# Performance work log

Hardware: AMD Instinct MI355X
Metric: run time of the kernel (lower is better)

The kernel has to match this reference:

```python
import jax, jax.numpy as jnp
import numpy as np

N = 50000
E0 = 800000
IN_CH = 128
HID = 64
OUT_CH = 64
HEADS = 2
NEG_SLOPE = 0.2


def _xavier(key, shape):
    fan_in, fan_out = shape[-2], shape[-1]
    limit = (6.0 / (fan_in + fan_out)) ** 0.5
    return jax.random.uniform(key, shape, jnp.float32, -limit, limit)


def setup_inputs() -> dict:
    key = jax.random.key(0)
    ks = jax.random.split(key, 10)
    x = jax.random.normal(ks[0], (N, IN_CH), jnp.float32)
    src = jax.random.randint(ks[1], (E0,), 0, N)
    dst = jax.random.randint(ks[2], (E0,), 0, N)
    dst = jnp.where(src == dst, (dst + 1) % N, dst)  # no self loops in input
    edge_index = jnp.stack([src, dst]).astype(jnp.int64)
    emb_w = _xavier(ks[3], (HID, IN_CH))
    emb_b = jnp.zeros((HID,), jnp.float32)
    # layer 0: in=HID, out=HID, heads=HEADS
    w0 = _xavier(ks[4], (HEADS, HID, HID))
    a0 = _xavier(ks[5], (1, HEADS, 2 * HID))
    # layer 1: in=HEADS*HID, out=HID, heads=HEADS
    w1 = _xavier(ks[6], (HEADS, HEADS * HID, HID))
    a1 = _xavier(ks[7], (1, HEADS, 2 * HID))
    # layer 2: in=HEADS*HID, out=OUT_CH, heads=1, concat=False
    w2 = _xavier(ks[8], (1, HEADS * HID, OUT_CH))
    a2 = _xavier(ks[9], (1, 1, 2 * OUT_CH))
    return {"x": x, "edge_index": edge_index, "emb_w": emb_w, "emb_b": emb_b,
            "w0": w0, "a0": a0, "w1": w1, "a1": a1, "w2": w2, "a2": a2}


def gat_layer(x, w, a, src, dst, concat):
    # x: [N, F_in]; w: [H, F_in, C]; a: [1, H, 2C]; src/dst: [E]
    C = w.shape[-1]
    xh = jnp.einsum('nf,hfc->nhc', x, w)               # [N, H, C]
    a_i, a_j = a[0, :, :C], a[0, :, C:]                # each [H, C]
    # (cat(x_i, x_j) * a).sum(-1) == <x_i, a_i> + <x_j, a_j>; compute per node then gather
    s_i = jnp.einsum('nhc,hc->nh', xh, a_i)            # [N, H]
    s_j = jnp.einsum('nhc,hc->nh', xh, a_j)            # [N, H]
    alpha = jax.nn.leaky_relu(s_i[dst] + s_j[src], NEG_SLOPE)  # [E, H]
    # segment softmax over destination nodes
    m = jax.ops.segment_max(alpha, dst, num_segments=N)
    alpha = jnp.exp(alpha - m[dst])
    denom = jax.ops.segment_sum(alpha, dst, num_segments=N)
    alpha = alpha / (denom[dst] + 1e-16)
    out = jax.ops.segment_sum(xh[src] * alpha[:, :, None], dst, num_segments=N)  # [N, H, C]
    if concat:
        return out.reshape(N, -1)
    return out.mean(axis=1)


def _forward(x, edge_index, emb_w, emb_b, w0, a0, w1, a1, w2, a2):
    # add self loops (inputs contain none, matching remove+add in the source)
    loop = jnp.arange(N, dtype=edge_index.dtype)
    src = jnp.concatenate([edge_index[0], loop])
    dst = jnp.concatenate([edge_index[1], loop])
    h = x @ emb_w.T + emb_b                            # nn.Linear embedding
    h = jax.nn.elu(gat_layer(h, w0, a0, src, dst, True))
    h = jax.nn.elu(gat_layer(h, w1, a1, src, dst, True))
    h = jax.nn.elu(gat_layer(h, w2, a2, src, dst, False))
    return h


def reference(x, edge_index, emb_w, emb_b, w0, a0, w1, a1, w2, a2):
    return _forward(x, edge_index, emb_w, emb_b, w0, a0, w1, a1, w2, a2)
```

## Files before the change

### kernel.cpp

```cpp
#include <hip/hip_runtime.h>
#include <math.h>

typedef __attribute__((ext_vector_type(8))) short short8v;
typedef __attribute__((ext_vector_type(4))) float float4v;

union uf32 { unsigned int u; float f; };

__device__ __forceinline__ unsigned short f2b(float f) {
  uf32 v; v.f = f;
  unsigned int u = v.u;
  return (unsigned short)((u + 0x7fffu + ((u >> 16) & 1u)) >> 16);
}

__global__ void zero8(int* __restrict__ p, int n) {
  int i = blockIdx.x * 256 + threadIdx.x;
  if (i < n) p[i] = 0;
}

__global__ void hist8(const int* __restrict__ ei, int* __restrict__ cnt8,
                      unsigned short* __restrict__ lpos, int E0, int N) {
  int e = blockIdx.x * 256 + threadIdx.x;
  if (e >= E0 + N) return;
  int vx = blockIdx.x & 7;
  int d = (e < E0) ? ei[E0 + e] : (e - E0);
  lpos[e] = (unsigned short)atomicAdd(&cnt8[vx * N + d], 1);
}

__global__ void fold8(const int* __restrict__ cnt8, int* __restrict__ base8,
                      int* __restrict__ cnt, int* __restrict__ part, int N) {
  __shared__ int lds[256];
  int d = blockIdx.x * 256 + threadIdx.x;
  int run = 0;
  if (d < N) {
#pragma unroll
    for (int x = 0; x < 8; ++x) {
      int t = cnt8[x * N + d];
      base8[x * N + d] = run;
      run += t;
    }
    cnt[d] = run;
  }
  lds[threadIdx.x] = (d < N) ? run : 0;
  __syncthreads();
  for (int o = 128; o; o >>= 1) {
    if (threadIdx.x < o) lds[threadIdx.x] += lds[threadIdx.x + o];
    __syncthreads();
  }
  if (threadIdx.x == 0) part[blockIdx.x] = lds[0];
}

__global__ void scan_carry(int* __restrict__ part, int nb) {
  __shared__ int lds[256];
  __shared__ int carry;
  if (threadIdx.x == 0) carry = 0;
  __syncthreads();
  for (int t0 = 0; t0 < nb; t0 += 256) {
    int t = t0 + threadIdx.x;
    int v = (t < nb) ? part[t] : 0;
    lds[threadIdx.x] = v;
    __syncthreads();
    for (int o = 1; o < 256; o <<= 1) {
      int x = (threadIdx.x >= o) ? lds[threadIdx.x - o] : 0;
      __syncthreads();
      lds[threadIdx.x] += x;
      __syncthreads();
    }
    if (t < nb) part[t] = carry + lds[threadIdx.x] - v;
    __syncthreads();
    if (threadIdx.x == 255) carry += lds[255];
    __syncthreads();
  }
}

__global__ void scan3(const int* __restrict__ cnt, const int* __restrict__ part,
                      const int* __restrict__ base8, int* __restrict__ rp,
                      int* __restrict__ rb8, int N, int E) {
  __shared__ int lds[256];
  int t = threadIdx.x;
  int idx = blockIdx.x * 256 + t;
  int v = (idx < N) ? cnt[idx] : 0;
  lds[t] = v;
  __syncthreads();
  for (int o = 1; o < 256; o <<= 1) {
    int x = (t >= o) ? lds[t - o] : 0;
    __syncthreads();
    lds[t] += x;
    __syncthreads();
  }
  if (idx < N) {
    const int rpv = part[blockIdx.x] + lds[t] - v;
    rp[idx] = rpv;
#pragma unroll
    for (int x = 0; x < 8; ++x) rb8[x * N + idx] = rpv + base8[x * N + idx];
  }
  if (blockIdx.x == 0 && t == 0) rp[N] = E;
}

__global__ void fillx(const int* __restrict__ ei, const int* __restrict__ rb8,
                      const unsigned short* __restrict__ lpos,
                      int* __restrict__ col, int E0, int N) {
  int e = blockIdx.x * 256 + threadIdx.x;
  if (e >= E0 + N) return;
  int vx = blockIdx.x & 7;
  int s, d;
  if (e < E0) { s = ei[e]; d = ei[E0 + e]; }
  else        { s = e - E0; d = s; }
  col[rb8[vx * N + d] + lpos[e]] = s;
}

__global__ void pack_all(const float* __restrict__ emb_w, const float* __restrict__ w0,
                         const float* __restrict__ w1, const float* __restrict__ w2,
                         unsigned short* __restrict__ pE, unsigned short* __restrict__ p0,
                         unsigned short* __restrict__ p1, unsigned short* __restrict__ p2) {
  int b = blockIdx.x;
  const float* w; unsigned short* bp;
  int F, sf, sc, h;
  if (b < 32)       { w = emb_w; bp = pE; F = 128; sf = 1;  sc = 128; h = 0; }
  else if (b < 64)  { b -= 32;  w = w0; bp = p0; F = 64;  sf = 64; sc = 1; h = b / 16; b %= 16; }
  else if (b < 128) { b -= 64;  w = w1; bp = p1; F = 128; sf = 64; sc = 1; h = b / 32; b %= 32; }
  else              { b -= 128; w = w2; bp = p2; F = 128; sf = 64; sc = 1; h = 0; }
  int i = b * 256 + threadIdx.x;
  if (i >= F * 64) return;
  int j = i & 7, colc = (i >> 3) & 15, g = (i >> 7) & 3, ct = (i >> 9) & 3, kk = i >> 11;
  int f = kk * 32 + g * 8 + j;
  int c = ct * 16 + colc;
  float v = w[(size_t)h * F * 64 + (size_t)f * sf + (size_t)c * sc];
  bp[(size_t)h * F * 64 + i] = f2b(v);
}

template <int F, int H, bool SCORES, bool BIAS, bool IBF, bool OBF>
__global__ __launch_bounds__(256) void gemm_mfma(
    const void* __restrict__ in, const unsigned short* __restrict__ bp,
    const float* __restrict__ bias, const float* __restrict__ a,
    void* __restrict__ xh_out, float* __restrict__ si, float* __restrict__ sj,
    int nrows) {
  constexpr int SA = F + 8;
  constexpr int NK = F / 32;
  constexpr int HC = H * 64;
  __shared__ __align__(16) unsigned short A_lds[64 * SA];

  const int tid = threadIdx.x;
  const int lane = tid & 63;
  const int wv = tid >> 6;
  const int n0 = blockIdx.x * 64;

  if (IBF) {
    const unsigned short* inb = (const unsigned short*)in;
    constexpr int NCH = 64 * F / 8;
#pragma unroll
    for (int i0 = 0; i0 < NCH; i0 += 256) {
      const int i = i0 + tid;
      const int row = i / (F / 8);
      const int c8 = i % (F / 8);
      int rg = n0 + row;
      if (rg >= nrows) rg = nrows - 1;
      const short8v v = *reinterpret_cast<const short8v*>(inb + (size_t)rg * F + c8 * 8);
      *reinterpret_cast<short8v*>(A_lds + row * SA + c8 * 8) = v;
    }
  } else {
    const float* inf = (const float*)in;
    constexpr int NCH = 64 * F / 4;
#pragma unroll
    for (int i0 = 0; i0 < NCH; i0 += 256) {
      const int i = i0 + tid;
      const int row = i / (F / 4);
      const int c4 = i % (F / 4);
      int rg = n0 + row;
      if (rg >= nrows) rg = nrows - 1;
      const float4 v = *reinterpret_cast<const float4*>(inf + (size_t)rg * F + c4 * 4);
      unsigned short* d = A_lds + row * SA + c4 * 4;
      d[0] = f2b(v.x); d[1] = f2b(v.y); d[2] = f2b(v.z); d[3] = f2b(v.w);
    }
  }
  __syncthreads();

  const int g = lane >> 4;
  const int cl = lane & 15;

  short8v af[NK];
  const unsigned short* ar = A_lds + (wv * 16 + cl) * SA + g * 8;
#pragma unroll
  for (int kk = 0; kk < NK; ++kk) af[kk] = *reinterpret_cast<const short8v*>(ar + kk * 32);

#pragma unroll
  for (int h = 0; h < H; ++h) {
    const unsigned short* __restrict__ bph = bp + (size_t)h * (F * 64);

    float4v acc[4];
#pragma unroll
    for (int ct = 0; ct < 4; ++ct) acc[ct] = (float4v){0.f, 0.f, 0.f, 0.f};

#pragma unroll
    for (int kk = 0; kk < NK; ++kk) {
#pragma unroll
      for (int ct = 0; ct < 4; ++ct) {
        const short8v bf = *reinterpret_cast<const short8v*>(
            bph + ((size_t)((kk * 4 + ct) * 4 + g)) * 128 + cl * 8);
        acc[ct] = __builtin_amdgcn_mfma_f32_16x16x32_bf16(af[kk], bf, acc[ct], 0, 0, 0);
      }
    }

    if (BIAS) {
#pragma unroll
      for (int ct = 0; ct < 4; ++ct) {
        const float b = bias[ct * 16 + cl];
#pragma unroll
        for (int reg = 0; reg < 4; ++reg) acc[ct][reg] += b;
      }
    }

#pragma unroll
    for (int ct = 0; ct < 4; ++ct) {
      const int c = ct * 16 + cl;
#pragma unroll
      for (int reg = 0; reg < 4; ++reg) {
        const int n = n0 + wv * 16 + g * 4 + reg;
        if (n < nrows) {
          const size_t idx = (size_t)n * HC + h * 64 + c;
          if (OBF) ((unsigned short*)xh_out)[idx] = f2b(acc[ct][reg]);
          else     ((float*)xh_out)[idx] = acc[ct][reg];
        }
      }
    }

    if (SCORES) {
      float pi[4] = {0.f, 0.f, 0.f, 0.f}, pj[4] = {0.f, 0.f, 0.f, 0.f};
#pragma unroll
      for (int ct = 0; ct < 4; ++ct) {
        const float av = a[h * 128 + ct * 16 + cl];
        const float bv = a[h * 128 + 64 + ct * 16 + cl];
#pragma unroll
        for (int reg = 0; reg < 4; ++reg) {
          pi[reg] = fmaf(acc[ct][reg], av, pi[reg]);
          pj[reg] = fmaf(acc[ct][reg], bv, pj[reg]);
        }
      }
#pragma unroll
      for (int reg = 0; reg < 4; ++reg) {
#pragma unroll
        for (int o = 8; o; o >>= 1) {
          pi[reg] += __shfl_xor(pi[reg], o, 64);
          pj[reg] += __shfl_xor(pj[reg], o, 64);
        }
      }
      if (cl == 0) {
#pragma unroll
        for (int reg = 0; reg < 4; ++reg) {
          const int n = n0 + wv * 16 + g * 4 + reg;
          if (n < nrows) {
            si[(size_t)n * H + h] = pi[reg];
            sj[(size_t)n * H + h] = pj[reg];
          }
        }
      }
    }
  }
}

template <int H, bool OBF>
__global__ __launch_bounds__(256) void agg_kernel(
    const unsigned short* __restrict__ xh, const float* __restrict__ si_g,
    const float* __restrict__ sj_g, const int* __restrict__ rp,
    const int* __restrict__ col, void* __restrict__ out, int N) {
  constexpr int HC = H * 64;
  const int lane = threadIdx.x & 63;
  const int n = blockIdx.x * 4 + (threadIdx.x >> 6);
  if (n >= N) return;
  const int el = lane & 31;
  const int hl = (H == 2) ? (lane >> 5) : 0;

  const int base = rp[n];
  const int deg = rp[n + 1] - base;
  const float siv = si_g[(size_t)n * H + hl];

  const int soff = (H == 1) ? (lane >> 5) : 0;
  const int qoff = (H == 1) ? (lane >> 5) : (lane & 32);
  constexpr int STEP = (H == 2) ? 1 : 2;
  const unsigned int loff = (H == 2) ? (unsigned)lane * 2 : (unsigned)el * 2;

  float m = 0.f, den = 0.f, acc0 = 0.f, acc1 = 0.f;

  for (int start = 0; start < deg; start += 32) {
    const int k = start + el;
    const bool vld = k < deg;
    const int s = vld ? col[base + k] : 0;
    float al = -INFINITY;
    if (vld) {
      const float t = siv + sj_g[(size_t)s * H + hl];
      al = (t > 0.f) ? t : 0.2f * t;
    }
    float cm = al;
#pragma unroll
    for (int o = 16; o; o >>= 1) cm = fmaxf(cm, __shfl_xor(cm, o, 64));
    if (start == 0) {
      m = cm;
    } else {
      const float nm = fmaxf(m, cm);
      const float r = __expf(m - nm);
      den *= r; acc0 *= r; acc1 *= r; m = nm;
    }
    const float p = vld ? __expf(al - m) : 0.f;
    float ps = p;
#pragma unroll
    for (int o = 16; o; o >>= 1) ps += __shfl_xor(ps, o, 64);
    den += ps;

    const int cc = min(32, deg - start);
    int kk = 0;
    for (; kk + 8 * STEP <= cc; kk += 8 * STEP) {
      int sb[8]; float qb[8]; unsigned int uv[8];
#pragma unroll
      for (int u = 0; u < 8; ++u) {
        const int e = kk + u * STEP;
        sb[u] = __shfl(s, e + soff, 64);
        qb[u] = __shfl(p, e + qoff, 64);
      }
#pragma unroll
      for (int u = 0; u < 8; ++u)
        uv[u] = *reinterpret_cast<const unsigned int*>(xh + (size_t)sb[u] * HC + loff);
#pragma unroll
      for (int u = 0; u < 8; ++u) {
        uf32 lo, hi;
        lo.u = uv[u] << 16;
        hi.u = uv[u] & 0xffff0000u;
        acc0 = fmaf(qb[u], lo.f, acc0);
        acc1 = fmaf(qb[u], hi.f, acc1);
      }
    }
    for (; kk + 4 * STEP <= cc; kk += 4 * STEP) {
      int sb[4]; float qb[4]; unsigned int uv[4];
#pragma unroll
      for (int u = 0; u < 4; ++u) {
        const int e = kk + u * STEP;
        sb[u] = __shfl(s, e + soff, 64);
        qb[u] = __shfl(p, e + qoff, 64);
      }
#pragma unroll
      for (int u = 0; u < 4; ++u)
        uv[u] = *reinterpret_cast<const unsigned int*>(xh + (size_t)sb[u] * HC + loff);
#pragma unroll
      for (int u = 0; u < 4; ++u) {
        uf32 lo, hi;
        lo.u = uv[u] << 16;
        hi.u = uv[u] & 0xffff0000u;
        acc0 = fmaf(qb[u], lo.f, acc0);
        acc1 = fmaf(qb[u], hi.f, acc1);
      }
    }
    for (; kk < cc; kk += STEP) {
      const int sb = __shfl(s, kk + soff, 64);
      const float qb = __shfl(p, kk + qoff, 64);
      const unsigned int uv = *reinterpret_cast<const unsigned int*>(xh + (size_t)sb * HC + loff);
      uf32 lo, hi;
      lo.u = uv << 16;
      hi.u = uv & 0xffff0000u;
      acc0 = fmaf(qb, lo.f, acc0);
      acc1 = fmaf(qb, hi.f, acc1);
    }
  }

  if (H == 2) {
    const float invd = 1.f / (den + 1e-16f);
    float v0 = acc0 * invd, v1 = acc1 * invd;
    v0 = (v0 > 0.f) ? v0 : expm1f(v0);
    v1 = (v1 > 0.f) ? v1 : expm1f(v1);
    if (OBF) {
      unsigned int pk = ((unsigned int)f2b(v1) << 16) | (unsigned int)f2b(v0);
      *reinterpret_cast<unsigned int*>((unsigned short*)out + (size_t)n * 128 + lane * 2) = pk;
    } else {
      float2 o; o.x = v0; o.y = v1;
      *reinterpret_cast<float2*>((float*)out + (size_t)n * 128 + lane * 2) = o;
    }
  } else {
    acc0 += __shfl_xor(acc0, 32, 64);
    acc1 += __shfl_xor(acc1, 32, 64);
    if (lane < 32) {
      const float invd = 1.f / (den + 1e-16f);
      float v0 = acc0 * invd, v1 = acc1 * invd;
      v0 = (v0 > 0.f) ? v0 : expm1f(v0);
      v1 = (v1 > 0.f) ? v1 : expm1f(v1);
      if (OBF) {
        unsigned int pk = ((unsigned int)f2b(v1) << 16) | (unsigned int)f2b(v0);
        *reinterpret_cast<unsigned int*>((unsigned short*)out + (size_t)n * 64 + el * 2) = pk;
      } else {
        float2 o; o.x = v0; o.y = v1;
        *reinterpret_cast<float2*>((float*)out + (size_t)n * 64 + el * 2) = o;
      }
    }
  }
}

extern "C" void kernel_launch(void* const* d_in, const int* in_sizes, int n_in,
                              void* d_out, int out_size, void* d_ws, size_t ws_size,
                              hipStream_t stream) {
  const float* x     = (const float*)d_in[0];
  const int*   ei    = (const int*)d_in[1];
  const float* emb_w = (const float*)d_in[2];
  const float* emb_b = (const float*)d_in[3];
  const float* w0    = (const float*)d_in[4];
  const float* a0    = (const float*)d_in[5];
  const float* w1    = (const float*)d_in[6];
  const float* a1    = (const float*)d_in[7];
  const float* w2    = (const float*)d_in[8];
  const float* a2    = (const float*)d_in[9];

  const int IN_CH = 128;
  int N  = in_sizes[0] / IN_CH;
  int E0 = in_sizes[1] / 2;
  int E  = E0 + N;

  char* p = (char*)d_ws;
  auto alloc = [&](size_t bytes) -> char* {
    char* r = p;
    p += (bytes + 255) & ~(size_t)255;
    return r;
  };
  unsigned short* hA  = (unsigned short*)alloc((size_t)N * 128 * 2);
  unsigned short* hB  = (unsigned short*)alloc((size_t)N * 128 * 2);
  unsigned short* xhb = (unsigned short*)alloc((size_t)N * 128 * 2);
  float* si   = (float*)alloc((size_t)N * 2 * 4);
  float* sj   = (float*)alloc((size_t)N * 2 * 4);
  unsigned short* packE = (unsigned short*)alloc(128 * 64 * 2);
  unsigned short* pack0 = (unsigned short*)alloc(2 * 64 * 64 * 2);
  unsigned short* pack1 = (unsigned short*)alloc(2 * 128 * 64 * 2);
  unsigned short* pack2 = (unsigned short*)alloc(128 * 64 * 2);
  int* rp    = (int*)alloc((size_t)(N + 1) * 4);
  int* cnt   = (int*)alloc((size_t)N * 4);
  int* cnt8  = (int*)alloc((size_t)8 * N * 4);
  int* base8 = (int*)alloc((size_t)8 * N * 4);
  int* rb8   = (int*)alloc((size_t)8 * N * 4);
  unsigned short* lpos = (unsigned short*)alloc((size_t)E * 2);
  int* col   = (int*)alloc((size_t)E * 4);
  int* part  = (int*)alloc(1024);

  dim3 blk(256);
  int gN = (N + 255) / 256;
  int gE = (E + 255) / 256;

  zero8<<<(8 * N + 255) / 256, blk, 0, stream>>>(cnt8, 8 * N);
  hist8<<<gE, blk, 0, stream>>>(ei, cnt8, lpos, E0, N);
  fold8<<<gN, blk, 0, stream>>>(cnt8, base8, cnt, part, N);
  scan_carry<<<1, blk, 0, stream>>>(part, gN);
  scan3<<<gN, blk, 0, stream>>>(cnt, part, base8, rp, rb8, N, E);
  fillx<<<gE, blk, 0, stream>>>(ei, rb8, lpos, col, E0, N);

  pack_all<<<160, blk, 0, stream>>>(emb_w, w0, w1, w2, packE, pack0, pack1, pack2);

  int gR = (N + 63) / 64;

  gemm_mfma<128, 1, false, true, false, true><<<gR, blk, 0, stream>>>(
      x, packE, emb_b, nullptr, hA, nullptr, nullptr, N);

  gemm_mfma<64, 2, true, false, true, true><<<gR, blk, 0, stream>>>(
      hA, pack0, nullptr, a0, xhb, si, sj, N);
  agg_kernel<2, true><<<(N + 3) / 4, blk, 0, stream>>>(xhb, si, sj, rp, col, hB, N);

  gemm_mfma<128, 2, true, false, true, true><<<gR, blk, 0, stream>>>(
      hB, pack1, nullptr, a1, xhb, si, sj, N);
  agg_kernel<2, true><<<(N + 3) / 4, blk, 0, stream>>>(xhb, si, sj, rp, col, hA, N);

  gemm_mfma<128, 1, true, false, true, true><<<gR, blk, 0, stream>>>(
      hA, pack2, nullptr, a2, xhb, si, sj, N);
  agg_kernel<1, false><<<(N + 3) / 4, blk, 0, stream>>>(xhb, si, sj, rp, col, (float*)d_out, N);
}
```

Baseline: 205.7 us.

## Fuse embedding and layer-0 GEMMs; stage aggregation indices in LDS

Merges the embedding linear layer and the layer-0 GAT projection into one kernel. The embedding result stays in shared memory as bf16 instead of round-tripping through global memory, which also removes a kernel launch. In the aggregation kernel, the per-edge source indices and softmax weights are written to per-wave LDS and read back as vectors, replacing many cross-lane shuffles. The LDS path adds a wave barrier and shortens the unroll from 8 to 4, which may reduce memory-level parallelism in the gathers.

```diff
diff --git a/kernel.cpp b/kernel.cpp
--- a/kernel.cpp
+++ b/kernel.cpp
@@ -128,12 +128,138 @@
   bp[(size_t)h * F * 64 + i] = f2b(v);
 }
 
-template <int F, int H, bool SCORES, bool BIAS, bool IBF, bool OBF>
+__global__ __launch_bounds__(256) void gemm_emb_l0(
+    const float* __restrict__ x, const unsigned short* __restrict__ packE,
+    const float* __restrict__ emb_b, const unsigned short* __restrict__ pack0,
+    const float* __restrict__ a0, unsigned short* __restrict__ xhb,
+    float* __restrict__ si, float* __restrict__ sj, int nrows) {
+  constexpr int SA = 136;
+  constexpr int SB = 72;
+  __shared__ __align__(16) unsigned short lds[64 * SA];
+
+  const int tid = threadIdx.x;
+  const int lane = tid & 63;
+  const int wv = tid >> 6;
+  const int n0 = blockIdx.x * 64;
+
+#pragma unroll
+  for (int i0 = 0; i0 < 64 * 32; i0 += 256) {
+    const int i = i0 + tid;
+    const int row = i >> 5, c4 = i & 31;
+    int rg = n0 + row;
+    if (rg >= nrows) rg = nrows - 1;
+    const float4 v = *reinterpret_cast<const float4*>(x + (size_t)rg * 128 + c4 * 4);
+    unsigned short* d = lds + row * SA + c4 * 4;
+    d[0] = f2b(v.x); d[1] = f2b(v.y); d[2] = f2b(v.z); d[3] = f2b(v.w);
+  }
+  __syncthreads();
+
+  const int g = lane >> 4;
+  const int cl = lane & 15;
+
+  short8v xf[4];
+  {
+    const unsigned short* ar = lds + (wv * 16 + cl) * SA + g * 8;
+#pragma unroll
+    for (int kk = 0; kk < 4; ++kk) xf[kk] = *reinterpret_cast<const short8v*>(ar + kk * 32);
+  }
+
+  float4v eacc[4];
+#pragma unroll
+  for (int ct = 0; ct < 4; ++ct) eacc[ct] = (float4v){0.f, 0.f, 0.f, 0.f};
+#pragma unroll
+  for (int kk = 0; kk < 4; ++kk) {
+#pragma unroll
+    for (int ct = 0; ct < 4; ++ct) {
+      const short8v bf = *reinterpret_cast<const short8v*>(
+          packE + ((size_t)((kk * 4 + ct) * 4 + g)) * 128 + cl * 8);
+      eacc[ct] = __builtin_amdgcn_mfma_f32_16x16x32_bf16(xf[kk], bf, eacc[ct], 0, 0, 0);
+    }
+  }
+  __syncthreads();
+
+#pragma unroll
+  for (int ct = 0; ct < 4; ++ct) {
+    const float b = emb_b[ct * 16 + cl];
+#pragma unroll
+    for (int reg = 0; reg < 4; ++reg) {
+      const int row = wv * 16 + g * 4 + reg;
+      lds[row * SB + ct * 16 + cl] = f2b(eacc[ct][reg] + b);
+    }
+  }
+  __syncthreads();
+
+  short8v af[2];
+  {
+    const unsigned short* ar2 = lds + (wv * 16 + cl) * SB + g * 8;
+#pragma unroll
+    for (int kk = 0; kk < 2; ++kk) af[kk] = *reinterpret_cast<const short8v*>(ar2 + kk * 32);
+  }
+
+#pragma unroll
+  for (int h = 0; h < 2; ++h) {
+    const unsigned short* __restrict__ bph = pack0 + (size_t)h * (64 * 64);
+
+    float4v acc[4];
+#pragma unroll
+    for (int ct = 0; ct < 4; ++ct) acc[ct] = (float4v){0.f, 0.f, 0.f, 0.f};
+#pragma unroll
+    for (int kk = 0; kk < 2; ++kk) {
+#pragma unroll
+      for (int ct = 0; ct < 4; ++ct) {
+        const short8v bf = *reinterpret_cast<const short8v*>(
+            bph + ((size_t)((kk * 4 + ct) * 4 + g)) * 128 + cl * 8);
+        acc[ct] = __builtin_amdgcn_mfma_f32_16x16x32_bf16(af[kk], bf, acc[ct], 0, 0, 0);
+      }
+    }
+
+#pragma unroll
+    for (int ct = 0; ct < 4; ++ct) {
+      const int c = ct * 16 + cl;
+#pragma unroll
+      for (int reg = 0; reg < 4; ++reg) {
+        const int n = n0 + wv * 16 + g * 4 + reg;
+        if (n < nrows) xhb[(size_t)n * 128 + h * 64 + c] = f2b(acc[ct][reg]);
+      }
+    }
+
+    float pi[4] = {0.f, 0.f, 0.f, 0.f}, pj[4] = {0.f, 0.f, 0.f, 0.f};
+#pragma unroll
+    for (int ct = 0; ct < 4; ++ct) {
+      const float av = a0[h * 128 + ct * 16 + cl];
+      const float bv = a0[h * 128 + 64 + ct * 16 + cl];
+#pragma unroll
+      for (int reg = 0; reg < 4; ++reg) {
+        pi[reg] = fmaf(acc[ct][reg], av, pi[reg]);
+        pj[reg] = fmaf(acc[ct][reg], bv, pj[reg]);
+      }
+    }
+#pragma unroll
+    for (int reg = 0; reg < 4; ++reg) {
+#pragma unroll
+      for (int o = 8; o; o >>= 1) {
+        pi[reg] += __shfl_xor(pi[reg], o, 64);
+        pj[reg] += __shfl_xor(pj[reg], o, 64);
+      }
+    }
+    if (cl == 0) {
+#pragma unroll
+      for (int reg = 0; reg < 4; ++reg) {
+        const int n = n0 + wv * 16 + g * 4 + reg;
+        if (n < nrows) {
+          si[(size_t)n * 2 + h] = pi[reg];
+          sj[(size_t)n * 2 + h] = pj[reg];
+        }
+      }
+    }
+  }
+}
+
+template <int F, int H, bool SCORES, bool OBF>
 __global__ __launch_bounds__(256) void gemm_mfma(
-    const void* __restrict__ in, const unsigned short* __restrict__ bp,
-    const float* __restrict__ bias, const float* __restrict__ a,
-    void* __restrict__ xh_out, float* __restrict__ si, float* __restrict__ sj,
-    int nrows) {
+    const unsigned short* __restrict__ in, const unsigned short* __restrict__ bp,
+    const float* __restrict__ a, void* __restrict__ xh_out,
+    float* __restrict__ si, float* __restrict__ sj, int nrows) {
   constexpr int SA = F + 8;
   constexpr int NK = F / 32;
   constexpr int HC = H * 64;
@@ -144,8 +270,7 @@
   const int wv = tid >> 6;
   const int n0 = blockIdx.x * 64;
 
-  if (IBF) {
-    const unsigned short* inb = (const unsigned short*)in;
+  {
     constexpr int NCH = 64 * F / 8;
 #pragma unroll
     for (int i0 = 0; i0 < NCH; i0 += 256) {
@@ -154,22 +279,8 @@
       const int c8 = i % (F / 8);
       int rg = n0 + row;
       if (rg >= nrows) rg = nrows - 1;
-      const short8v v = *reinterpret_cast<const short8v*>(inb + (size_t)rg * F + c8 * 8);
+      const short8v v = *reinterpret_cast<const short8v*>(in + (size_t)rg * F + c8 * 8);
       *reinterpret_cast<short8v*>(A_lds + row * SA + c8 * 8) = v;
-    }
-  } else {
-    const float* inf = (const float*)in;
-    constexpr int NCH = 64 * F / 4;
-#pragma unroll
-    for (int i0 = 0; i0 < NCH; i0 += 256) {
-      const int i = i0 + tid;
-      const int row = i / (F / 4);
-      const int c4 = i % (F / 4);
-      int rg = n0 + row;
-      if (rg >= nrows) rg = nrows - 1;
-      const float4 v = *reinterpret_cast<const float4*>(inf + (size_t)rg * F + c4 * 4);
-      unsigned short* d = A_lds + row * SA + c4 * 4;
-      d[0] = f2b(v.x); d[1] = f2b(v.y); d[2] = f2b(v.z); d[3] = f2b(v.w);
     }
   }
   __syncthreads();
@@ -197,15 +308,6 @@
         const short8v bf = *reinterpret_cast<const short8v*>(
             bph + ((size_t)((kk * 4 + ct) * 4 + g)) * 128 + cl * 8);
         acc[ct] = __builtin_amdgcn_mfma_f32_16x16x32_bf16(af[kk], bf, acc[ct], 0, 0, 0);
-      }
-    }
-
-    if (BIAS) {
-#pragma unroll
-      for (int ct = 0; ct < 4; ++ct) {
-        const float b = bias[ct * 16 + cl];
-#pragma unroll
-        for (int reg = 0; reg < 4; ++reg) acc[ct][reg] += b;
       }
     }
 
@@ -263,19 +365,25 @@
     const float* __restrict__ sj_g, const int* __restrict__ rp,
     const int* __restrict__ col, void* __restrict__ out, int N) {
   constexpr int HC = H * 64;
+  __shared__ __align__(16) int s_lds_all[4][32];
+  __shared__ __align__(16) float p_lds_all[4][2][40];
+
   const int lane = threadIdx.x & 63;
-  const int n = blockIdx.x * 4 + (threadIdx.x >> 6);
+  const int wv = threadIdx.x >> 6;
+  const int n = blockIdx.x * 4 + wv;
   if (n >= N) return;
   const int el = lane & 31;
-  const int hl = (H == 2) ? (lane >> 5) : 0;
+  const int half = lane >> 5;
+  const int hl = (H == 2) ? half : 0;
+
+  int* s_lds = s_lds_all[wv];
+  float* p_lds = p_lds_all[wv][0];
+  const int pbase = (H == 2) ? hl * 40 : 0;
 
   const int base = rp[n];
   const int deg = rp[n + 1] - base;
   const float siv = si_g[(size_t)n * H + hl];
 
-  const int soff = (H == 1) ? (lane >> 5) : 0;
-  const int qoff = (H == 1) ? (lane >> 5) : (lane & 32);
-  constexpr int STEP = (H == 2) ? 1 : 2;
   const unsigned int loff = (H == 2) ? (unsigned)lane * 2 : (unsigned)el * 2;
 
   float m = 0.f, den = 0.f, acc0 = 0.f, acc1 = 0.f;
@@ -305,57 +413,72 @@
     for (int o = 16; o; o >>= 1) ps += __shfl_xor(ps, o, 64);
     den += ps;
 
+    if (lane < 32) s_lds[el] = s;
+    p_lds[pbase + el] = p;
+    __builtin_amdgcn_wave_barrier();
+
     const int cc = min(32, deg - start);
     int kk = 0;
-    for (; kk + 8 * STEP <= cc; kk += 8 * STEP) {
-      int sb[8]; float qb[8]; unsigned int uv[8];
-#pragma unroll
-      for (int u = 0; u < 8; ++u) {
-        const int e = kk + u * STEP;
-        sb[u] = __shfl(s, e + soff, 64);
-        qb[u] = __shfl(p, e + qoff, 64);
-      }
-#pragma unroll
-      for (int u = 0; u < 8; ++u)
-        uv[u] = *reinterpret_cast<const unsigned int*>(xh + (size_t)sb[u] * HC + loff);
-#pragma unroll
-      for (int u = 0; u < 8; ++u) {
+    if (H == 2) {
+      for (; kk + 4 <= cc; kk += 4) {
+        const int4 sv = *reinterpret_cast<const int4*>(&s_lds[kk]);
+        const float4 qv = *reinterpret_cast<const float4*>(&p_lds[pbase + kk]);
+        unsigned int uv[4];
+        uv[0] = *reinterpret_cast<const unsigned int*>(xh + (size_t)sv.x * HC + loff);
+        uv[1] = *reinterpret_cast<const unsigned int*>(xh + (size_t)sv.y * HC + loff);
+        uv[2] = *reinterpret_cast<const unsigned int*>(xh + (size_t)sv.z * HC + loff);
+        uv[3] = *reinterpret_cast<const unsigned int*>(xh + (size_t)sv.w * HC + loff);
+        const float qs[4] = {qv.x, qv.y, qv.z, qv.w};
+#pragma unroll
+        for (int u = 0; u < 4; ++u) {
+          uf32 lo, hi;
+          lo.u = uv[u] << 16;
+          hi.u = uv[u] & 0xffff0000u;
+          acc0 = fmaf(qs[u], lo.f, acc0);
+          acc1 = fmaf(qs[u], hi.f, acc1);
+        }
+      }
+      for (; kk < cc; ++kk) {
+        const int sb = s_lds[kk];
+        const float qb = p_lds[pbase + kk];
+        const unsigned int uv = *reinterpret_cast<const unsigned int*>(xh + (size_t)sb * HC + loff);
         uf32 lo, hi;
-        lo.u = uv[u] << 16;
-        hi.u = uv[u] & 0xffff0000u;
-        acc0 = fmaf(qb[u], lo.f, acc0);
-        acc1 = fmaf(qb[u], hi.f, acc1);
-      }
-    }
-    for (; kk + 4 * STEP <= cc; kk += 4 * STEP) {
-      int sb[4]; float qb[4]; unsigned int uv[4];
-#pragma unroll
-      for (int u = 0; u < 4; ++u) {
-        const int e = kk + u * STEP;
-        sb[u] = __shfl(s, e + soff, 64);
-        qb[u] = __shfl(p, e + qoff, 64);
-      }
-#pragma unroll
-      for (int u = 0; u < 4; ++u)
-        uv[u] = *reinterpret_cast<const unsigned int*>(xh + (size_t)sb[u] * HC + loff);
-#pragma unroll
-      for (int u = 0; u < 4; ++u) {
+        lo.u = uv << 16;
+        hi.u = uv & 0xffff0000u;
+        acc0 = fmaf(qb, lo.f, acc0);
+        acc1 = fmaf(qb, hi.f, acc1);
+      }
+    } else {
+      for (; kk + 4 <= cc; kk += 4) {
+        const int4 sv = *reinterpret_cast<const int4*>(&s_lds[kk]);
+        const float4 qv = *reinterpret_cast<const float4*>(&p_lds[kk]);
+        const int sA = half ? sv.y : sv.x;
+        const int sB = half ? sv.w : sv.z;
+        const float qA = half ? qv.y : qv.x;
+        const float qB = half ? qv.w : qv.z;
+        const unsigned int uvA = *reinterpret_cast<const unsigned int*>(xh + (size_t)sA * HC + loff);
+        const unsigned int uvB = *reinterpret_cast<const unsigned int*>(xh + (size_t)sB * HC + loff);
         uf32 lo, hi;
-        lo.u = uv[u] << 16;
-        hi.u = uv[u] & 0xffff0000u;
-        acc0 = fmaf(qb[u], lo.f, acc0);
-        acc1 = fmaf(qb[u], hi.f, acc1);
-      }
-    }
-    for (; kk < cc; kk += STEP) {
-      const int sb = __shfl(s, kk + soff, 64);
-      const float qb = __shfl(p, kk + qoff, 64);
-      const unsigned int uv = *reinterpret_cast<const unsigned int*>(xh + (size_t)sb * HC + loff);
-      uf32 lo, hi;
-      lo.u = uv << 16;
-      hi.u = uv & 0xffff0000u;
-      acc0 = fmaf(qb, lo.f, acc0);
-      acc1 = fmaf(qb, hi.f, acc1);
+        lo.u = uvA << 16; hi.u = uvA & 0xffff0000u;
+        acc0 = fmaf(qA, lo.f, acc0);
+        acc1 = fmaf(qA, hi.f, acc1);
+        lo.u = uvB << 16; hi.u = uvB & 0xffff0000u;
+        acc0 = fmaf(qB, lo.f, acc0);
+        acc1 = fmaf(qB, hi.f, acc1);
+      }
+      for (; kk < cc; kk += 2) {
+        const int e = kk + half;
+        if (e < cc) {
+          const int sb = s_lds[e];
+          const float qb = p_lds[e];
+          const unsigned int uv = *reinterpret_cast<const unsigned int*>(xh + (size_t)sb * HC + loff);
+          uf32 lo, hi;
+          lo.u = uv << 16;
+          hi.u = uv & 0xffff0000u;
+          acc0 = fmaf(qb, lo.f, acc0);
+          acc1 = fmaf(qb, hi.f, acc1);
+        }
+      }
     }
   }
 
@@ -448,18 +571,12 @@
 
   int gR = (N + 63) / 64;
 
-  gemm_mfma<128, 1, false, true, false, true><<<gR, blk, 0, stream>>>(
-      x, packE, emb_b, nullptr, hA, nullptr, nullptr, N);
-
-  gemm_mfma<64, 2, true, false, true, true><<<gR, blk, 0, stream>>>(
-      hA, pack0, nullptr, a0, xhb, si, sj, N);
+  gemm_emb_l0<<<gR, blk, 0, stream>>>(x, packE, emb_b, pack0, a0, xhb, si, sj, N);
   agg_kernel<2, true><<<(N + 3) / 4, blk, 0, stream>>>(xhb, si, sj, rp, col, hB, N);
 
-  gemm_mfma<128, 2, true, false, true, true><<<gR, blk, 0, stream>>>(
-      hB, pack1, nullptr, a1, xhb, si, sj, N);
+  gemm_mfma<128, 2, true, true><<<gR, blk, 0, stream>>>(hB, pack1, a1, xhb, si, sj, N);
   agg_kernel<2, true><<<(N + 3) / 4, blk, 0, stream>>>(xhb, si, sj, rp, col, hA, N);
 
-  gemm_mfma<128, 1, true, false, true, true><<<gR, blk, 0, stream>>>(
-      hA, pack2, nullptr, a2, xhb, si, sj, N);
+  gemm_mfma<128, 1, true, true><<<gR, blk, 0, stream>>>(hA, pack2, a2, xhb, si, sj, N);
   agg_kernel<1, false><<<(N + 3) / 4, blk, 0, stream>>>(xhb, si, sj, rp, col, (float*)d_out, N);
 }
```

Result: slower. 210.3 us (+2.2%).
